# Optimization experiments

Measured on AMD Instinct MI355X. Metric: run time of the kernel, lower is better.

The kernel has to match this reference:

```python
import jax, jax.numpy as jnp
import numpy as np
import math

H = 8  # n_heads

def rel_shift(x):
    # x: [B, H, U, P] -> Transformer-XL relative shift
    B, h, U, P = x.shape
    x = jnp.pad(x, ((0, 0), (0, 0), (0, 0), (1, 0)))  # zero-pad front of last dim
    x = x.reshape(B, h, P + 1, U)[:, :, 1:, :].reshape(B, h, U, P)
    return x

def setup_inputs() -> dict:
    key = jax.random.key(0)
    ks = jax.random.split(key, 16)
    B, T, D = 8, 1024, 512
    s = 0.05  # weight scale ~ xavier for D=512
    inp = {
        'q': jax.random.normal(ks[0], (B, T, D), jnp.float32),
        'k': jax.random.normal(ks[1], (B, T, D), jnp.float32),
        'v': jax.random.normal(ks[2], (B, T, D), jnp.float32),
        'pos': jax.random.normal(ks[3], (T, D), jnp.float32),
        'mask': jax.random.randint(ks[4], (B, T, T), 0, 2).astype(jnp.int32),
        'Wq': jax.random.normal(ks[5], (D, D), jnp.float32) * s,
        'bq': jnp.zeros((D,), jnp.float32),
        'Wk': jax.random.normal(ks[6], (D, D), jnp.float32) * s,
        'bk': jnp.zeros((D,), jnp.float32),
        'Wv': jax.random.normal(ks[7], (D, D), jnp.float32) * s,
        'bv': jnp.zeros((D,), jnp.float32),
        'Wo': jax.random.normal(ks[8], (D, D), jnp.float32) * s,
        'bo': jnp.zeros((D,), jnp.float32),
        'Wp': jax.random.normal(ks[9], (D, D), jnp.float32) * s,
        'bias_u': jax.random.normal(ks[10], (H, D // H), jnp.float32) * s,
        'bias_v': jax.random.normal(ks[11], (H, D // H), jnp.float32) * s,
    }
    return inp

def reference(q, k, v, pos, mask, Wq, bq, Wk, bk, Wv, bv, Wo, bo, Wp, bias_u, bias_v):
    B, T, D = q.shape
    dk = D // H
    qh = (q @ Wq.T + bq).reshape(B, T, H, dk)   # B U H d
    kh = (k @ Wk.T + bk).reshape(B, T, H, dk)   # B T H d
    vh = (v @ Wv.T + bv).reshape(B, T, H, dk)   # B T H d
    ph = (pos @ Wp.T).reshape(T, H, dk)          # P H d (shared across batch)
    q_u = qh + bias_u                            # B U H d
    q_v = qh + bias_v
    ac = jnp.einsum('buhd,bthd->bhut', q_u, kh)  # content term
    bd = jnp.einsum('buhd,phd->bhup', q_v, ph)   # position term
    bd = rel_shift(bd)[:, :, :, :T]
    scores = (ac + bd) / math.sqrt(dk)           # B H U T
    m = (mask[:, None, :, :] == 0)               # B 1 U T
    neg = jnp.finfo(scores.dtype).min
    scores = jnp.where(m, neg, scores)
    attn = jax.nn.softmax(scores, axis=-1)
    attn = jnp.where(m, 0.0, attn)
    x = jnp.einsum('bhut,bthd->buhd', attn, vh).reshape(B, T, D)
    return x @ Wo.T + bo
```

## Files before the change

### kernel.cpp

```cpp
#include <hip/hip_runtime.h>
#include <stdint.h>

#define Bc 8
#define Tc 1024
#define Dc 512
#define Hc 8

typedef __bf16 bf16x8 __attribute__((ext_vector_type(8)));
typedef float f32x4 __attribute__((ext_vector_type(4)));
typedef unsigned short ushort8v __attribute__((ext_vector_type(8)));

__device__ __forceinline__ unsigned short f2bf(float f) {
    union { float f; uint32_t u; } v; v.f = f;
    uint32_t u = v.u;
    u += 0x7fffu + ((u >> 16) & 1u);
    return (unsigned short)(u >> 16);
}
__device__ __forceinline__ float bf2f(unsigned short s) {
    union { uint32_t u; float f; } v; v.u = ((uint32_t)s) << 16;
    return v.f;
}
__device__ __forceinline__ unsigned short f2bf_native(float f) {
    __bf16 b = (__bf16)f;
    return *(unsigned short*)&b;
}
__device__ __forceinline__ f32x4 mfma16(bf16x8 a, bf16x8 b, f32x4 c) {
    return __builtin_amdgcn_mfma_f32_16x16x32_bf16(a, b, c, 0, 0, 0);
}

__global__ __launch_bounds__(256) void pack_prep(
    const int* __restrict__ mask, uint32_t* __restrict__ bits,
    const float* __restrict__ Wq, const float* __restrict__ Wk,
    const float* __restrict__ Wv, const float* __restrict__ Wp,
    const float* __restrict__ Wo, unsigned short* __restrict__ Wb)
{
    int bid = blockIdx.x;
    if (bid < 32768) {
        int wid = (bid * 256 + threadIdx.x) >> 6;
        int lane = threadIdx.x & 63;
        unsigned long long bl = __ballot(mask[(size_t)wid * 64 + lane] != 0);
        if (lane == 0)  bits[wid * 2]     = (uint32_t)bl;
        if (lane == 32) bits[wid * 2 + 1] = (uint32_t)(bl >> 32);
    } else {
        int i = (bid - 32768) * 2048 + threadIdx.x * 8;
        int m = i >> 18, r = i & 262143;
        const float* Ws[5] = {Wq, Wk, Wv, Wp, Wo};
        const float* s = Ws[m] + r;
        ushort8v o;
#pragma unroll
        for (int j = 0; j < 8; ++j) o[j] = f2bf(s[j]);
        *(ushort8v*)(Wb + i) = o;
    }
}

__global__ __launch_bounds__(256) void proj4(
    const float* __restrict__ qin, const float* __restrict__ kin,
    const float* __restrict__ vin, const float* __restrict__ pin,
    const unsigned short* __restrict__ Wb,
    const float* __restrict__ bq, const float* __restrict__ bk,
    const float* __restrict__ bv,
    const float* __restrict__ bias_u, const float* __restrict__ bias_v,
    unsigned short* __restrict__ qu, unsigned short* __restrict__ qv,
    unsigned short* __restrict__ kh, unsigned short* __restrict__ vT,
    unsigned short* __restrict__ ph)
{
    const int z = blockIdx.z;
    if (z == 3 && blockIdx.y >= 8) return;
    const float* A = z == 0 ? qin : z == 1 ? kin : z == 2 ? vin : pin;
    const unsigned short* W = Wb + (size_t)z * 262144;

    const int n0 = blockIdx.y * 128, m0 = blockIdx.x * 128;
    __shared__ unsigned short As[128][72];
    __shared__ unsigned short Bs[128][72];
    const int tid = threadIdx.x, lane = tid & 63, wave = tid >> 6;
    const int lrow = lane & 15, lkg = lane >> 4;
    const int wr = (wave >> 1) * 64, wc = (wave & 1) * 64;

    f32x4 acc[4][4];
#pragma unroll
    for (int i = 0; i < 4; ++i)
#pragma unroll
        for (int j = 0; j < 4; ++j) acc[i][j] = f32x4{0.f, 0.f, 0.f, 0.f};

    for (int kt = 0; kt < 512; kt += 64) {
        __syncthreads();
#pragma unroll
        for (int it = 0; it < 4; ++it) {
            int c = tid + it * 256;
            int r = c >> 3, kc = (c & 7) * 8;
            const float* src = A + (size_t)(n0 + r) * 512 + kt + kc;
            ushort8v v;
#pragma unroll
            for (int j = 0; j < 8; ++j) v[j] = f2bf(src[j]);
            *(ushort8v*)&As[r][kc] = v;
            *(ushort8v*)&Bs[r][kc] =
                *(const ushort8v*)(W + (size_t)(m0 + r) * 512 + kt + kc);
        }
        __syncthreads();
#pragma unroll
        for (int kk = 0; kk < 2; ++kk) {
            bf16x8 a[4], bb[4];
#pragma unroll
            for (int i = 0; i < 4; ++i)
                a[i] = *(const bf16x8*)&As[wr + i * 16 + lrow][kk * 32 + lkg * 8];
#pragma unroll
            for (int j = 0; j < 4; ++j)
                bb[j] = *(const bf16x8*)&Bs[wc + j * 16 + lrow][kk * 32 + lkg * 8];
#pragma unroll
            for (int i = 0; i < 4; ++i)
#pragma unroll
                for (int j = 0; j < 4; ++j)
                    acc[i][j] = mfma16(a[i], bb[j], acc[i][j]);
        }
    }

#pragma unroll
    for (int i = 0; i < 4; ++i) {
        int nbase = n0 + wr + i * 16 + lkg * 4;
#pragma unroll
        for (int j = 0; j < 4; ++j) {
            int m = m0 + wc + j * 16 + lrow;
            float bb = z == 0 ? bq[m] : z == 1 ? bk[m] : z == 2 ? bv[m] : 0.f;
            float bu = 0.f, bvv = 0.f;
            if (z == 0) { bu = bias_u[m]; bvv = bias_v[m]; }
#pragma unroll
            for (int q = 0; q < 4; ++q) {
                int n = nbase + q;
                float c = acc[i][j][q] + bb;
                if (z == 0) {
                    qu[(size_t)n * 512 + m] = f2bf(c + bu);
                    qv[(size_t)n * 512 + m] = f2bf(c + bvv);
                } else if (z == 1) {
                    kh[(size_t)n * 512 + m] = f2bf(c);
                } else if (z == 2) {
                    int b = n >> 10, t = n & 1023, h = m >> 6, d = m & 63;
                    vT[(((size_t)((b * 8 + h) * 64 + d)) << 10) + t] = f2bf(c);
                } else {
                    ph[(size_t)n * 512 + m] = f2bf(c);
                }
            }
        }
    }
}

__global__ __launch_bounds__(256) void gemm_out(
    const unsigned short* __restrict__ X, const unsigned short* __restrict__ Wob,
    const float* __restrict__ bo, float* __restrict__ fout)
{
    const int n0 = blockIdx.y * 128, m0 = blockIdx.x * 128;
    __shared__ unsigned short As[128][72];
    __shared__ unsigned short Bs[128][72];
    const int tid = threadIdx.x, lane = tid & 63, wave = tid >> 6;
    const int lrow = lane & 15, lkg = lane >> 4;
    const int wr = (wave >> 1) * 64, wc = (wave & 1) * 64;

    f32x4 acc[4][4];
#pragma unroll
    for (int i = 0; i < 4; ++i)
#pragma unroll
        for (int j = 0; j < 4; ++j) acc[i][j] = f32x4{0.f, 0.f, 0.f, 0.f};

    for (int kt = 0; kt < 512; kt += 64) {
        __syncthreads();
#pragma unroll
        for (int it = 0; it < 4; ++it) {
            int c = tid + it * 256;
            int r = c >> 3, kc = (c & 7) * 8;
            *(ushort8v*)&As[r][kc] =
                *(const ushort8v*)(X + (size_t)(n0 + r) * 512 + kt + kc);
            *(ushort8v*)&Bs[r][kc] =
                *(const ushort8v*)(Wob + (size_t)(m0 + r) * 512 + kt + kc);
        }
        __syncthreads();
#pragma unroll
        for (int kk = 0; kk < 2; ++kk) {
            bf16x8 a[4], bb[4];
#pragma unroll
            for (int i = 0; i < 4; ++i)
                a[i] = *(const bf16x8*)&As[wr + i * 16 + lrow][kk * 32 + lkg * 8];
#pragma unroll
            for (int j = 0; j < 4; ++j)
                bb[j] = *(const bf16x8*)&Bs[wc + j * 16 + lrow][kk * 32 + lkg * 8];
#pragma unroll
            for (int i = 0; i < 4; ++i)
#pragma unroll
                for (int j = 0; j < 4; ++j)
                    acc[i][j] = mfma16(a[i], bb[j], acc[i][j]);
        }
    }
#pragma unroll
    for (int i = 0; i < 4; ++i) {
        int nbase = n0 + wr + i * 16 + lkg * 4;
#pragma unroll
        for (int j = 0; j < 4; ++j) {
            int m = m0 + wc + j * 16 + lrow;
            float bb = bo[m];
#pragma unroll
            for (int q = 0; q < 4; ++q)
                fout[(size_t)(nbase + q) * 512 + m] = acc[i][j][q] + bb;
        }
    }
}

__global__ __launch_bounds__(256) void bd_gemm(
    const unsigned short* __restrict__ qv, const unsigned short* __restrict__ ph,
    unsigned short* __restrict__ bds, int bh_base)
{
    const int u0 = blockIdx.x * 128, p0 = blockIdx.y * 128;
    const int bh = bh_base + blockIdx.z;
    const int b = bh >> 3, h = bh & 7;
    __shared__ unsigned short As[128][72];
    __shared__ unsigned short Bs[128][72];
    const int tid = threadIdx.x, lane = tid & 63, wave = tid >> 6;
    const int lrow = lane & 15, lkg = lane >> 4;
    const int wr = (wave >> 1) * 64, wc = (wave & 1) * 64;

#pragma unroll
    for (int it = 0; it < 4; ++it) {
        int c = tid + it * 256;
        int r = c >> 3, kc = (c & 7) * 8;
        *(ushort8v*)&As[r][kc] =
            *(const ushort8v*)(qv + ((size_t)(b * 1024 + u0 + r)) * 512 + h * 64 + kc);
        *(ushort8v*)&Bs[r][kc] =
            *(const ushort8v*)(ph + ((size_t)(p0 + r)) * 512 + h * 64 + kc);
    }
    __syncthreads();

    f32x4 acc[4][4];
#pragma unroll
    for (int i = 0; i < 4; ++i)
#pragma unroll
        for (int j = 0; j < 4; ++j) acc[i][j] = f32x4{0.f, 0.f, 0.f, 0.f};
#pragma unroll
    for (int kk = 0; kk < 2; ++kk) {
        bf16x8 a[4], bb[4];
#pragma unroll
        for (int i = 0; i < 4; ++i)
            a[i] = *(const bf16x8*)&As[wr + i * 16 + lrow][kk * 32 + lkg * 8];
#pragma unroll
        for (int j = 0; j < 4; ++j)
            bb[j] = *(const bf16x8*)&Bs[wc + j * 16 + lrow][kk * 32 + lkg * 8];
#pragma unroll
        for (int i = 0; i < 4; ++i)
#pragma unroll
            for (int j = 0; j < 4; ++j)
                acc[i][j] = mfma16(a[i], bb[j], acc[i][j]);
    }

    unsigned short* dst = bds + ((size_t)blockIdx.z << 20);
#pragma unroll
    for (int i = 0; i < 4; ++i) {
#pragma unroll
        for (int j = 0; j < 4; ++j) {
#pragma unroll
            for (int q = 0; q < 4; ++q) {
                int u = u0 + wr + i * 16 + lkg * 4 + q;
                int p = p0 + wc + j * 16 + lrow;
                unsigned short val = f2bf(acc[i][j][q] * 0.125f);
                if (p >= 1023 - u) {
                    dst[((size_t)u << 10) + (p + u - 1023)] = val;
                } else if (u >= 1) {
                    dst[((size_t)(u - 1) << 10) + (p + u + 1)] = val;
                }
            }
        }
    }
}

__global__ __launch_bounds__(256, 4) void attn3(
    const unsigned short* __restrict__ qu, const unsigned short* __restrict__ kh,
    const unsigned short* __restrict__ vT, const unsigned short* __restrict__ bds,
    const uint32_t* __restrict__ mbits, unsigned short* __restrict__ xout,
    int b_base)
{
    int id = blockIdx.x, nid, b, rem;
    if (gridDim.x == 1024) {
        nid = (id & 7) * 128 + (id >> 3);
        b = b_base + (nid >> 7); rem = nid & 127;
    } else {
        nid = (id & 7) * 16 + (id >> 3);
        b = b_base; rem = nid;
    }
    const int h = rem >> 4, ublk = rem & 15;
    const int u0 = ublk * 64;

    __shared__ unsigned short Ks[64][72];
    __shared__ unsigned short Vs[64][72];
    __shared__ unsigned short Ps[4][16][72];
    __shared__ uint32_t Mw[64][32];
    const int tid = threadIdx.x, lane = tid & 63, wave = tid >> 6;
    const int lrow = lane & 15, lkg = lane >> 4;
    const f32x4 zero = {0.f, 0.f, 0.f, 0.f};

    {
        const uint32_t* src = mbits + ((size_t)(b * 1024 + u0)) * 32;
        ((uint4*)Mw)[tid]       = ((const uint4*)src)[tid];
        ((uint4*)Mw)[tid + 256] = ((const uint4*)src)[tid + 256];
    }

    const unsigned short* qub = qu + ((size_t)(b * 1024 + u0 + wave * 16 + lrow)) * 512 + h * 64;
    bf16x8 au0 = *(const bf16x8*)(qub + lkg * 8);
    bf16x8 au1 = *(const bf16x8*)(qub + 32 + lkg * 8);

    const int urow = u0 + wave * 16 + lkg * 4;
    const int zoff = (b - b_base) * 8 + h;
    const unsigned short* bdb = bds + ((size_t)zoff << 20);
    const unsigned short* kbase = kh + ((size_t)(b * 1024)) * 512 + h * 64;
    const unsigned short* vbase = vT + (((size_t)((b * 8 + h) * 64)) << 10);

    f32x4 acc[4] = {zero, zero, zero, zero};
    float mrow[4], lsum[4];
#pragma unroll
    for (int q = 0; q < 4; ++q) { mrow[q] = -3.0e38f; lsum[q] = 0.f; }

    for (int t0 = 0; t0 < 1024; t0 += 64) {
        __syncthreads();
        {
            int r = tid >> 3, c8 = (tid & 7) * 8;
            *(ushort8v*)&Ks[r][c8]      = *(const ushort8v*)(kbase + (size_t)(t0 + r) * 512 + c8);
            *(ushort8v*)&Ks[r + 32][c8] = *(const ushort8v*)(kbase + (size_t)(t0 + r + 32) * 512 + c8);
            *(ushort8v*)&Vs[r][c8]      = *(const ushort8v*)(vbase + ((size_t)r << 10) + t0 + c8);
            *(ushort8v*)&Vs[r + 32][c8] = *(const ushort8v*)(vbase + ((size_t)(r + 32) << 10) + t0 + c8);
        }
        float bdv[4][4];
#pragma unroll
        for (int j = 0; j < 4; ++j) {
            int t = t0 + j * 16 + lrow;
#pragma unroll
            for (int q = 0; q < 4; ++q) {
                int u = urow + q;
                float v = bf2f(bdb[((size_t)u << 10) + t]);
                bdv[j][q] = (t == u + 1) ? 0.f : v;
            }
        }
        __syncthreads();
        uint32_t mw0[4], mw1[4];
#pragma unroll
        for (int q = 0; q < 4; ++q) {
            mw0[q] = Mw[urow + q - u0][t0 >> 5];
            mw1[q] = Mw[urow + q - u0][(t0 >> 5) + 1];
        }

        f32x4 s[4];
#pragma unroll
        for (int j = 0; j < 4; ++j) {
            bf16x8 k0 = *(const bf16x8*)&Ks[j * 16 + lrow][lkg * 8];
            bf16x8 k1 = *(const bf16x8*)&Ks[j * 16 + lrow][32 + lkg * 8];
            s[j] = mfma16(au1, k1, mfma16(au0, k0, zero));
        }
#pragma unroll
        for (int j = 0; j < 4; ++j) {
#pragma unroll
            for (int q = 0; q < 4; ++q) {
                float sv = fmaf(s[j][q], 0.125f, bdv[j][q]);
                uint32_t w = (j < 2) ? mw0[q] : mw1[q];
                if (!((w >> ((j & 1) * 16 + lrow)) & 1)) sv = -1.0e30f;
                s[j][q] = sv;
            }
        }
        float lmax[4];
#pragma unroll
        for (int q = 0; q < 4; ++q)
            lmax[q] = fmaxf(fmaxf(s[0][q], s[1][q]), fmaxf(s[2][q], s[3][q]));
        int need = (lmax[0] > mrow[0] + 8.f) | (lmax[1] > mrow[1] + 8.f) |
                   (lmax[2] > mrow[2] + 8.f) | (lmax[3] > mrow[3] + 8.f);
        if (__any(need)) {
            float rmx[4] = {lmax[0], lmax[1], lmax[2], lmax[3]};
#pragma unroll
            for (int off = 1; off < 16; off <<= 1)
#pragma unroll
                for (int q = 0; q < 4; ++q) rmx[q] = fmaxf(rmx[q], __shfl_xor(rmx[q], off));
#pragma unroll
            for (int q = 0; q < 4; ++q) {
                float mn = fmaxf(mrow[q], rmx[q]);
                float fr = __expf(mrow[q] - mn);
                mrow[q] = mn;
                lsum[q] *= fr;
#pragma unroll
                for (int jj = 0; jj < 4; ++jj) acc[jj][q] *= fr;
            }
        }
#pragma unroll
        for (int j = 0; j < 4; ++j) {
#pragma unroll
            for (int q = 0; q < 4; ++q) {
                float p = __expf(s[j][q] - mrow[q]);
                lsum[q] += p;
                Ps[wave][lkg * 4 + q][j * 16 + lrow] = f2bf_native(p);
            }
        }
        bf16x8 pa0 = *(const bf16x8*)&Ps[wave][lrow][lkg * 8];
        bf16x8 pa1 = *(const bf16x8*)&Ps[wave][lrow][32 + lkg * 8];
#pragma unroll
        for (int jj = 0; jj < 4; ++jj) {
            bf16x8 vb0 = *(const bf16x8*)&Vs[jj * 16 + lrow][lkg * 8];
            bf16x8 vb1 = *(const bf16x8*)&Vs[jj * 16 + lrow][32 + lkg * 8];
            acc[jj] = mfma16(pa1, vb1, mfma16(pa0, vb0, acc[jj]));
        }
    }

#pragma unroll
    for (int off = 1; off < 16; off <<= 1)
#pragma unroll
        for (int q = 0; q < 4; ++q) lsum[q] += __shfl_xor(lsum[q], off);
#pragma unroll
    for (int q = 0; q < 4; ++q) {
        float inv = 1.0f / lsum[q];
        int u = urow + q;
#pragma unroll
        for (int jj = 0; jj < 4; ++jj) {
            int d = jj * 16 + lrow;
            xout[((size_t)(b * 1024 + u)) * 512 + h * 64 + d] = f2bf_native(acc[jj][q] * inv);
        }
    }
}

extern "C" void kernel_launch(void* const* d_in, const int* in_sizes, int n_in,
                              void* d_out, int out_size, void* d_ws, size_t ws_size,
                              hipStream_t stream) {
    const float* q    = (const float*)d_in[0];
    const float* k    = (const float*)d_in[1];
    const float* v    = (const float*)d_in[2];
    const float* pos  = (const float*)d_in[3];
    const int*   mask = (const int*)d_in[4];
    const float* Wq   = (const float*)d_in[5];
    const float* bq   = (const float*)d_in[6];
    const float* Wk   = (const float*)d_in[7];
    const float* bk   = (const float*)d_in[8];
    const float* Wv   = (const float*)d_in[9];
    const float* bv   = (const float*)d_in[10];
    const float* Wo   = (const float*)d_in[11];
    const float* bo   = (const float*)d_in[12];
    const float* Wp   = (const float*)d_in[13];
    const float* bias_u = (const float*)d_in[14];
    const float* bias_v = (const float*)d_in[15];
    float* out = (float*)d_out;

    unsigned short* ws = (unsigned short*)d_ws;
    constexpr size_t NQ  = (size_t)Bc * Tc * Dc;
    constexpr size_t NP  = (size_t)Tc * Dc;
    constexpr size_t NMB = (size_t)Bc * Tc * 32;
    constexpr size_t NWB = (size_t)5 * 262144;
    unsigned short* ws_qu = ws;
    unsigned short* ws_qv = ws_qu + NQ;
    unsigned short* ws_kh = ws_qv + NQ;
    unsigned short* ws_vT = ws_kh + NQ;
    unsigned short* ws_ph = ws_vT + NQ;
    uint32_t*       ws_mb = (uint32_t*)(ws_ph + NP);
    unsigned short* ws_wb = (unsigned short*)(ws_mb + NMB);
    unsigned short* ws_bd = ws_wb + NWB;

    constexpr size_t BD_FULL  = (size_t)64 * 1024 * 1024;
    constexpr size_t BD_SMALL = (size_t)8 * 1024 * 1024;
    const size_t base_bytes = (4 * NQ + NP + NWB) * 2 + NMB * 4;
    const bool full  = ws_size >= base_bytes + BD_FULL * 2;
    const bool tier2 = !full && ws_size >= base_bytes + (BD_SMALL + NQ) * 2;

    dim3 blk(256);
    pack_prep<<<33408, blk, 0, stream>>>(mask, ws_mb, Wq, Wk, Wv, Wp, Wo, ws_wb);
    proj4<<<dim3(4, 64, 4), blk, 0, stream>>>(q, k, v, pos, ws_wb, bq, bk, bv,
                                              bias_u, bias_v, ws_qu, ws_qv, ws_kh, ws_vT, ws_ph);

    if (full) {
        unsigned short* ws_x = ws_qv;
        bd_gemm<<<dim3(8, 8, 64), blk, 0, stream>>>(ws_qv, ws_ph, ws_bd, 0);
        attn3<<<dim3(1024), blk, 0, stream>>>(ws_qu, ws_kh, ws_vT, ws_bd, ws_mb, ws_x, 0);
        gemm_out<<<dim3(4, 64), blk, 0, stream>>>(ws_x, ws_wb + 4 * 262144, bo, out);
    } else if (tier2) {
        unsigned short* ws_x = ws_bd + BD_SMALL;
        for (int b = 0; b < 8; ++b) {
            bd_gemm<<<dim3(8, 8, 8), blk, 0, stream>>>(ws_qv, ws_ph, ws_bd, b * 8);
            attn3<<<dim3(128), blk, 0, stream>>>(ws_qu, ws_kh, ws_vT, ws_bd, ws_mb, ws_x, b);
        }
        gemm_out<<<dim3(4, 64), blk, 0, stream>>>(ws_x, ws_wb + 4 * 262144, bo, out);
    }
}
```

Measured before the change: 212.0 us.

## Pre-convert inputs to bf16, use direct global-to-LDS loads, remap block order, exp2 softmax

The prep kernel now converts q, k, v and pos to bf16 in a separate pass, so the projection GEMM loads bf16 tiles straight into LDS with global_load_lds instead of converting in registers. All GEMM-style kernels and the attention K/V tile loads switch to 16-byte direct global-to-LDS copies, which means dropping the LDS row padding and accepting possible bank conflicts. Grids become 1D with a modulo-8 block remap, apparently to spread work across XCDs. Softmax folds log2(e) into the scale constant and uses exp2f, and the extra bf16 buffers alias the bd workspace.

Result: slower. 217.0 us (+2.3%).

```diff
diff --git a/kernel.cpp b/kernel.cpp
--- a/kernel.cpp
+++ b/kernel.cpp
@@ -27,12 +27,24 @@
 __device__ __forceinline__ f32x4 mfma16(bf16x8 a, bf16x8 b, f32x4 c) {
     return __builtin_amdgcn_mfma_f32_16x16x32_bf16(a, b, c, 0, 0, 0);
 }
-
-__global__ __launch_bounds__(256) void pack_prep(
+__device__ __forceinline__ void gl16(const unsigned short* g, unsigned short* l) {
+    __builtin_amdgcn_global_load_lds(
+        (const __attribute__((address_space(1))) uint32_t*)g,
+        (__attribute__((address_space(3))) uint32_t*)l, 16, 0, 0);
+}
+
+#define SC2 0.1803368801f
+#define THR2 11.541560327f
+
+__global__ __launch_bounds__(256) void prep(
     const int* __restrict__ mask, uint32_t* __restrict__ bits,
     const float* __restrict__ Wq, const float* __restrict__ Wk,
     const float* __restrict__ Wv, const float* __restrict__ Wp,
-    const float* __restrict__ Wo, unsigned short* __restrict__ Wb)
+    const float* __restrict__ Wo, unsigned short* __restrict__ Wb,
+    const float* __restrict__ q, const float* __restrict__ k,
+    const float* __restrict__ v, const float* __restrict__ p,
+    unsigned short* __restrict__ qb, unsigned short* __restrict__ kb,
+    unsigned short* __restrict__ vb, unsigned short* __restrict__ pb)
 {
     int bid = blockIdx.x;
     if (bid < 32768) {
@@ -41,7 +53,7 @@
         unsigned long long bl = __ballot(mask[(size_t)wid * 64 + lane] != 0);
         if (lane == 0)  bits[wid * 2]     = (uint32_t)bl;
         if (lane == 32) bits[wid * 2 + 1] = (uint32_t)(bl >> 32);
-    } else {
+    } else if (bid < 33408) {
         int i = (bid - 32768) * 2048 + threadIdx.x * 8;
         int m = i >> 18, r = i & 262143;
         const float* Ws[5] = {Wq, Wk, Wv, Wp, Wo};
@@ -50,12 +62,23 @@
 #pragma unroll
         for (int j = 0; j < 8; ++j) o[j] = f2bf(s[j]);
         *(ushort8v*)(Wb + i) = o;
+    } else {
+        size_t i = (size_t)(bid - 33408) * 2048 + threadIdx.x * 8;
+        const float* src; unsigned short* dst; size_t off;
+        if (i < 4194304)       { src = q; dst = qb; off = i; }
+        else if (i < 8388608)  { src = k; dst = kb; off = i - 4194304; }
+        else if (i < 12582912) { src = v; dst = vb; off = i - 8388608; }
+        else                   { src = p; dst = pb; off = i - 12582912; }
+        ushort8v o;
+#pragma unroll
+        for (int j = 0; j < 8; ++j) o[j] = f2bf(src[off + j]);
+        *(ushort8v*)(dst + off) = o;
     }
 }
 
 __global__ __launch_bounds__(256) void proj4(
-    const float* __restrict__ qin, const float* __restrict__ kin,
-    const float* __restrict__ vin, const float* __restrict__ pin,
+    const unsigned short* __restrict__ qb, const unsigned short* __restrict__ kb,
+    const unsigned short* __restrict__ vb, const unsigned short* __restrict__ pb,
     const unsigned short* __restrict__ Wb,
     const float* __restrict__ bq, const float* __restrict__ bk,
     const float* __restrict__ bv,
@@ -64,17 +87,23 @@
     unsigned short* __restrict__ kh, unsigned short* __restrict__ vT,
     unsigned short* __restrict__ ph)
 {
-    const int z = blockIdx.z;
-    if (z == 3 && blockIdx.y >= 8) return;
-    const float* A = z == 0 ? qin : z == 1 ? kin : z == 2 ? vin : pin;
+    int id = blockIdx.x;
+    int wg = (id & 7) * 100 + (id >> 3);
+    int z, rem;
+    if (wg < 256)      { z = 0; rem = wg; }
+    else if (wg < 512) { z = 1; rem = wg - 256; }
+    else if (wg < 768) { z = 2; rem = wg - 512; }
+    else               { z = 3; rem = wg - 768; }
+    const int m0 = (rem & 3) * 128, n0 = (rem >> 2) * 128;
+    const unsigned short* A = z == 0 ? qb : z == 1 ? kb : z == 2 ? vb : pb;
     const unsigned short* W = Wb + (size_t)z * 262144;
 
-    const int n0 = blockIdx.y * 128, m0 = blockIdx.x * 128;
-    __shared__ unsigned short As[128][72];
-    __shared__ unsigned short Bs[128][72];
+    __shared__ unsigned short As[128][64];
+    __shared__ unsigned short Bs[128][64];
     const int tid = threadIdx.x, lane = tid & 63, wave = tid >> 6;
     const int lrow = lane & 15, lkg = lane >> 4;
     const int wr = (wave >> 1) * 64, wc = (wave & 1) * 64;
+    const int srow = lane >> 3, scol = (lane & 7) * 8;
 
     f32x4 acc[4][4];
 #pragma unroll
@@ -86,15 +115,9 @@
         __syncthreads();
 #pragma unroll
         for (int it = 0; it < 4; ++it) {
-            int c = tid + it * 256;
-            int r = c >> 3, kc = (c & 7) * 8;
-            const float* src = A + (size_t)(n0 + r) * 512 + kt + kc;
-            ushort8v v;
-#pragma unroll
-            for (int j = 0; j < 8; ++j) v[j] = f2bf(src[j]);
-            *(ushort8v*)&As[r][kc] = v;
-            *(ushort8v*)&Bs[r][kc] =
-                *(const ushort8v*)(W + (size_t)(m0 + r) * 512 + kt + kc);
+            int r8 = (wave * 4 + it) * 8;
+            gl16(A + (size_t)(n0 + r8 + srow) * 512 + kt + scol, &As[r8][0]);
+            gl16(W + (size_t)(m0 + r8 + srow) * 512 + kt + scol, &Bs[r8][0]);
         }
         __syncthreads();
 #pragma unroll
@@ -124,9 +147,9 @@
             float bu = 0.f, bvv = 0.f;
             if (z == 0) { bu = bias_u[m]; bvv = bias_v[m]; }
 #pragma unroll
-            for (int q = 0; q < 4; ++q) {
-                int n = nbase + q;
-                float c = acc[i][j][q] + bb;
+            for (int qq = 0; qq < 4; ++qq) {
+                int n = nbase + qq;
+                float c = acc[i][j][qq] + bb;
                 if (z == 0) {
                     qu[(size_t)n * 512 + m] = f2bf(c + bu);
                     qv[(size_t)n * 512 + m] = f2bf(c + bvv);
@@ -147,12 +170,15 @@
     const unsigned short* __restrict__ X, const unsigned short* __restrict__ Wob,
     const float* __restrict__ bo, float* __restrict__ fout)
 {
-    const int n0 = blockIdx.y * 128, m0 = blockIdx.x * 128;
-    __shared__ unsigned short As[128][72];
-    __shared__ unsigned short Bs[128][72];
+    int id = blockIdx.x;
+    int wg = (id & 7) * 32 + (id >> 3);
+    const int m0 = (wg & 3) * 128, n0 = (wg >> 2) * 128;
+    __shared__ unsigned short As[128][64];
+    __shared__ unsigned short Bs[128][64];
     const int tid = threadIdx.x, lane = tid & 63, wave = tid >> 6;
     const int lrow = lane & 15, lkg = lane >> 4;
     const int wr = (wave >> 1) * 64, wc = (wave & 1) * 64;
+    const int srow = lane >> 3, scol = (lane & 7) * 8;
 
     f32x4 acc[4][4];
 #pragma unroll
@@ -164,12 +190,9 @@
         __syncthreads();
 #pragma unroll
         for (int it = 0; it < 4; ++it) {
-            int c = tid + it * 256;
-            int r = c >> 3, kc = (c & 7) * 8;
-            *(ushort8v*)&As[r][kc] =
-                *(const ushort8v*)(X + (size_t)(n0 + r) * 512 + kt + kc);
-            *(ushort8v*)&Bs[r][kc] =
-                *(const ushort8v*)(Wob + (size_t)(m0 + r) * 512 + kt + kc);
+            int r8 = (wave * 4 + it) * 8;
+            gl16(X   + (size_t)(n0 + r8 + srow) * 512 + kt + scol, &As[r8][0]);
+            gl16(Wob + (size_t)(m0 + r8 + srow) * 512 + kt + scol, &Bs[r8][0]);
         }
         __syncthreads();
 #pragma unroll
@@ -196,8 +219,8 @@
             int m = m0 + wc + j * 16 + lrow;
             float bb = bo[m];
 #pragma unroll
-            for (int q = 0; q < 4; ++q)
-                fout[(size_t)(nbase + q) * 512 + m] = acc[i][j][q] + bb;
+            for (int qq = 0; qq < 4; ++qq)
+                fout[(size_t)(nbase + qq) * 512 + m] = acc[i][j][qq] + bb;
         }
     }
 }
@@ -206,23 +229,25 @@
     const unsigned short* __restrict__ qv, const unsigned short* __restrict__ ph,
     unsigned short* __restrict__ bds, int bh_base)
 {
-    const int u0 = blockIdx.x * 128, p0 = blockIdx.y * 128;
-    const int bh = bh_base + blockIdx.z;
+    int id = blockIdx.x, wg;
+    if (gridDim.x == 4096) wg = (id & 7) * 512 + (id >> 3);
+    else                   wg = (id & 7) * 64 + (id >> 3);
+    const int zz = wg >> 6, rem = wg & 63;
+    const int u0 = (rem & 7) * 128, p0 = (rem >> 3) * 128;
+    const int bh = bh_base + zz;
     const int b = bh >> 3, h = bh & 7;
-    __shared__ unsigned short As[128][72];
-    __shared__ unsigned short Bs[128][72];
+    __shared__ unsigned short As[128][64];
+    __shared__ unsigned short Bs[128][64];
     const int tid = threadIdx.x, lane = tid & 63, wave = tid >> 6;
     const int lrow = lane & 15, lkg = lane >> 4;
     const int wr = (wave >> 1) * 64, wc = (wave & 1) * 64;
+    const int srow = lane >> 3, scol = (lane & 7) * 8;
 
 #pragma unroll
     for (int it = 0; it < 4; ++it) {
-        int c = tid + it * 256;
-        int r = c >> 3, kc = (c & 7) * 8;
-        *(ushort8v*)&As[r][kc] =
-            *(const ushort8v*)(qv + ((size_t)(b * 1024 + u0 + r)) * 512 + h * 64 + kc);
-        *(ushort8v*)&Bs[r][kc] =
-            *(const ushort8v*)(ph + ((size_t)(p0 + r)) * 512 + h * 64 + kc);
+        int r8 = (wave * 4 + it) * 8;
+        gl16(qv + ((size_t)(b * 1024 + u0 + r8 + srow)) * 512 + h * 64 + scol, &As[r8][0]);
+        gl16(ph + ((size_t)(p0 + r8 + srow)) * 512 + h * 64 + scol, &Bs[r8][0]);
     }
     __syncthreads();
 
@@ -247,16 +272,16 @@
                 acc[i][j] = mfma16(a[i], bb[j], acc[i][j]);
     }
 
-    unsigned short* dst = bds + ((size_t)blockIdx.z << 20);
+    unsigned short* dst = bds + ((size_t)zz << 20);
 #pragma unroll
     for (int i = 0; i < 4; ++i) {
 #pragma unroll
         for (int j = 0; j < 4; ++j) {
 #pragma unroll
-            for (int q = 0; q < 4; ++q) {
-                int u = u0 + wr + i * 16 + lkg * 4 + q;
+            for (int qq = 0; qq < 4; ++qq) {
+                int u = u0 + wr + i * 16 + lkg * 4 + qq;
                 int p = p0 + wc + j * 16 + lrow;
-                unsigned short val = f2bf(acc[i][j][q] * 0.125f);
+                unsigned short val = f2bf(acc[i][j][qq] * SC2);
                 if (p >= 1023 - u) {
                     dst[((size_t)u << 10) + (p + u - 1023)] = val;
                 } else if (u >= 1) {
@@ -267,7 +292,7 @@
     }
 }
 
-__global__ __launch_bounds__(256, 4) void attn3(
+__global__ __launch_bounds__(256, 4) void attn4(
     const unsigned short* __restrict__ qu, const unsigned short* __restrict__ kh,
     const unsigned short* __restrict__ vT, const unsigned short* __restrict__ bds,
     const uint32_t* __restrict__ mbits, unsigned short* __restrict__ xout,
@@ -284,12 +309,13 @@
     const int h = rem >> 4, ublk = rem & 15;
     const int u0 = ublk * 64;
 
-    __shared__ unsigned short Ks[64][72];
-    __shared__ unsigned short Vs[64][72];
+    __shared__ unsigned short Ks[64][64];
+    __shared__ unsigned short Vs[64][64];
     __shared__ unsigned short Ps[4][16][72];
     __shared__ uint32_t Mw[64][32];
     const int tid = threadIdx.x, lane = tid & 63, wave = tid >> 6;
     const int lrow = lane & 15, lkg = lane >> 4;
+    const int srow = lane >> 3, scol = (lane & 7) * 8;
     const f32x4 zero = {0.f, 0.f, 0.f, 0.f};
 
     {
@@ -315,12 +341,11 @@
 
     for (int t0 = 0; t0 < 1024; t0 += 64) {
         __syncthreads();
-        {
-            int r = tid >> 3, c8 = (tid & 7) * 8;
-            *(ushort8v*)&Ks[r][c8]      = *(const ushort8v*)(kbase + (size_t)(t0 + r) * 512 + c8);
-            *(ushort8v*)&Ks[r + 32][c8] = *(const ushort8v*)(kbase + (size_t)(t0 + r + 32) * 512 + c8);
-            *(ushort8v*)&Vs[r][c8]      = *(const ushort8v*)(vbase + ((size_t)r << 10) + t0 + c8);
-            *(ushort8v*)&Vs[r + 32][c8] = *(const ushort8v*)(vbase + ((size_t)(r + 32) << 10) + t0 + c8);
+#pragma unroll
+        for (int it = 0; it < 2; ++it) {
+            int r8 = (wave * 2 + it) * 8;
+            gl16(kbase + (size_t)(t0 + r8 + srow) * 512 + scol, &Ks[r8][0]);
+            gl16(vbase + ((size_t)(r8 + srow) << 10) + t0 + scol, &Vs[r8][0]);
         }
         float bdv[4][4];
 #pragma unroll
@@ -334,12 +359,10 @@
             }
         }
         __syncthreads();
-        uint32_t mw0[4], mw1[4];
-#pragma unroll
-        for (int q = 0; q < 4; ++q) {
-            mw0[q] = Mw[urow + q - u0][t0 >> 5];
-            mw1[q] = Mw[urow + q - u0][(t0 >> 5) + 1];
-        }
+        uint32_t mw[4][2];
+#pragma unroll
+        for (int q = 0; q < 4; ++q)
+            *(uint2*)&mw[q][0] = *(const uint2*)&Mw[urow + q - u0][t0 >> 5];
 
         f32x4 s[4];
 #pragma unroll
@@ -352,9 +375,8 @@
         for (int j = 0; j < 4; ++j) {
 #pragma unroll
             for (int q = 0; q < 4; ++q) {
-                float sv = fmaf(s[j][q], 0.125f, bdv[j][q]);
-                uint32_t w = (j < 2) ? mw0[q] : mw1[q];
-                if (!((w >> ((j & 1) * 16 + lrow)) & 1)) sv = -1.0e30f;
+                float sv = fmaf(s[j][q], SC2, bdv[j][q]);
+                if (!((mw[q][j >> 1] >> ((j & 1) * 16 + lrow)) & 1)) sv = -1.0e30f;
                 s[j][q] = sv;
             }
         }
@@ -362,8 +384,8 @@
 #pragma unroll
         for (int q = 0; q < 4; ++q)
             lmax[q] = fmaxf(fmaxf(s[0][q], s[1][q]), fmaxf(s[2][q], s[3][q]));
-        int need = (lmax[0] > mrow[0] + 8.f) | (lmax[1] > mrow[1] + 8.f) |
-                   (lmax[2] > mrow[2] + 8.f) | (lmax[3] > mrow[3] + 8.f);
+        int need = (lmax[0] > mrow[0] + THR2) | (lmax[1] > mrow[1] + THR2) |
+                   (lmax[2] > mrow[2] + THR2) | (lmax[3] > mrow[3] + THR2);
         if (__any(need)) {
             float rmx[4] = {lmax[0], lmax[1], lmax[2], lmax[3]};
 #pragma unroll
@@ -373,7 +395,7 @@
 #pragma unroll
             for (int q = 0; q < 4; ++q) {
                 float mn = fmaxf(mrow[q], rmx[q]);
-                float fr = __expf(mrow[q] - mn);
+                float fr = exp2f(mrow[q] - mn);
                 mrow[q] = mn;
                 lsum[q] *= fr;
 #pragma unroll
@@ -384,7 +406,7 @@
         for (int j = 0; j < 4; ++j) {
 #pragma unroll
             for (int q = 0; q < 4; ++q) {
-                float p = __expf(s[j][q] - mrow[q]);
+                float p = exp2f(s[j][q] - mrow[q]);
                 lsum[q] += p;
                 Ps[wave][lkg * 4 + q][j * 16 + lrow] = f2bf_native(p);
             }
@@ -448,30 +470,35 @@
     unsigned short* ws_ph = ws_vT + NQ;
     uint32_t*       ws_mb = (uint32_t*)(ws_ph + NP);
     unsigned short* ws_wb = (unsigned short*)(ws_mb + NMB);
-    unsigned short* ws_bd = ws_wb + NWB;
+    unsigned short* ws_qb = ws_wb + NWB;
+    unsigned short* ws_kb = ws_qb + NQ;
+    unsigned short* ws_vb = ws_kb + NQ;
+    unsigned short* ws_pb = ws_vb + NQ;
+    unsigned short* ws_bd = ws_qb;
 
     constexpr size_t BD_FULL  = (size_t)64 * 1024 * 1024;
     constexpr size_t BD_SMALL = (size_t)8 * 1024 * 1024;
     const size_t base_bytes = (4 * NQ + NP + NWB) * 2 + NMB * 4;
     const bool full  = ws_size >= base_bytes + BD_FULL * 2;
-    const bool tier2 = !full && ws_size >= base_bytes + (BD_SMALL + NQ) * 2;
+    const bool tier2 = !full && ws_size >= base_bytes + ((3 * NQ + NP) + NQ) * 2;
 
     dim3 blk(256);
-    pack_prep<<<33408, blk, 0, stream>>>(mask, ws_mb, Wq, Wk, Wv, Wp, Wo, ws_wb);
-    proj4<<<dim3(4, 64, 4), blk, 0, stream>>>(q, k, v, pos, ws_wb, bq, bk, bv,
-                                              bias_u, bias_v, ws_qu, ws_qv, ws_kh, ws_vT, ws_ph);
+    prep<<<39808, blk, 0, stream>>>(mask, ws_mb, Wq, Wk, Wv, Wp, Wo, ws_wb,
+                                    q, k, v, pos, ws_qb, ws_kb, ws_vb, ws_pb);
+    proj4<<<800, blk, 0, stream>>>(ws_qb, ws_kb, ws_vb, ws_pb, ws_wb, bq, bk, bv,
+                                   bias_u, bias_v, ws_qu, ws_qv, ws_kh, ws_vT, ws_ph);
 
     if (full) {
         unsigned short* ws_x = ws_qv;
-        bd_gemm<<<dim3(8, 8, 64), blk, 0, stream>>>(ws_qv, ws_ph, ws_bd, 0);
-        attn3<<<dim3(1024), blk, 0, stream>>>(ws_qu, ws_kh, ws_vT, ws_bd, ws_mb, ws_x, 0);
-        gemm_out<<<dim3(4, 64), blk, 0, stream>>>(ws_x, ws_wb + 4 * 262144, bo, out);
+        bd_gemm<<<4096, blk, 0, stream>>>(ws_qv, ws_ph, ws_bd, 0);
+        attn4<<<1024, blk, 0, stream>>>(ws_qu, ws_kh, ws_vT, ws_bd, ws_mb, ws_x, 0);
+        gemm_out<<<256, blk, 0, stream>>>(ws_x, ws_wb + 4 * 262144, bo, out);
     } else if (tier2) {
-        unsigned short* ws_x = ws_bd + BD_SMALL;
+        unsigned short* ws_x = ws_qb + 3 * NQ + NP;
         for (int b = 0; b < 8; ++b) {
-            bd_gemm<<<dim3(8, 8, 8), blk, 0, stream>>>(ws_qv, ws_ph, ws_bd, b * 8);
-            attn3<<<dim3(128), blk, 0, stream>>>(ws_qu, ws_kh, ws_vT, ws_bd, ws_mb, ws_x, b);
-        }
-        gemm_out<<<dim3(4, 64), blk, 0, stream>>>(ws_x, ws_wb + 4 * 262144, bo, out);
-    }
-}
+            bd_gemm<<<512, blk, 0, stream>>>(ws_qv, ws_ph, ws_bd, b * 8);
+            attn4<<<128, blk, 0, stream>>>(ws_qu, ws_kh, ws_vT, ws_bd, ws_mb, ws_x, b);
+        }
+        gemm_out<<<256, blk, 0, stream>>>(ws_x, ws_wb + 4 * 262144, bo, out);
+    }
+}
```
